# Performance work log

Hardware: AMD Instinct MI355X
Metric: run time of the kernel (lower is better)

Reference implementation:

```python
import jax, jax.numpy as jnp
import numpy as np

B, T, D = 4, 50, 512
SRC, SENTS, WORDS = 400, 16, 40
NEG = jnp.float32(-1e30)  # stands in for -inf mask fill (numerically identical post-softmax)


def _seq_mask(lengths, max_len):
    # [n, max_len] bool, True where position < length
    return jnp.arange(max_len)[None, :] < lengths[:, None]


def _mlp_score(q, h, Wq, bq, Uc, v):
    # Bahdanau additive score: v^T tanh(W q + U h)
    # q: [b,t,d], h: [b,s,d] -> [b,t,s]
    wq = q @ Wq + bq                       # [b,t,d]
    uh = h @ Uc                            # [b,s,d]
    wquh = jnp.tanh(wq[:, :, None, :] + uh[:, None, :, :])  # [b,t,s,d]
    return jnp.einsum('btsd,d->bts', wquh, v)


def setup_inputs() -> dict:
    key = jax.random.key(0)
    ks = jax.random.split(key, 20)
    s = np.float32(1.0 / np.sqrt(D))
    def p(k, shape):
        return jax.random.normal(k, shape, jnp.float32) * s
    return {
        'source': jax.random.normal(ks[0], (B, T, D), jnp.float32),
        'src_bank': jax.random.normal(ks[1], (SRC, B, D), jnp.float32),
        'src_lengths': jax.random.randint(ks[2], (B,), 1, SRC + 1),
        'qa_sent_bank': jax.random.normal(ks[3], (SENTS, B, D), jnp.float32),
        'qa_sent_lengths': jax.random.randint(ks[4], (B,), 1, SENTS + 1),
        'qa_word_bank': jax.random.normal(ks[5], (WORDS, B, SENTS, D), jnp.float32),
        'qa_word_lengths': jax.random.randint(ks[6], (B, SENTS), 1, WORDS + 1),
        'Wq_word': p(ks[7], (D, D)), 'bq_word': jnp.zeros((D,), jnp.float32),
        'Uc_word': p(ks[8], (D, D)), 'v_word': p(ks[9], (D,)),
        'Wq_sent': p(ks[10], (D, D)), 'bq_sent': jnp.zeros((D,), jnp.float32),
        'Uc_sent': p(ks[11], (D, D)), 'v_sent': p(ks[12], (D,)),
        'Wq_pass': p(ks[13], (D, D)), 'bq_pass': jnp.zeros((D,), jnp.float32),
        'Uc_pass': p(ks[14], (D, D)), 'v_pass': p(ks[15], (D,)),
    }


def _forward(source, src_bank, qa_sent_bank, qa_word_bank,
             Wq_word, bq_word, Uc_word, v_word,
             Wq_sent, bq_sent, Uc_sent, v_sent,
             Wq_pass, bq_pass, Uc_pass, v_pass,
             src_lengths, qa_word_lengths):
    b = source.shape[0]
    # [words,b,sents,d] -> [b,sents,words,d] -> [b, sents*words, d]
    qa_word = jnp.transpose(qa_word_bank, (1, 2, 0, 3)).reshape(b, SENTS * WORDS, D)
    src = jnp.transpose(src_bank, (1, 0, 2))       # [b,src,d]
    sent = jnp.transpose(qa_sent_bank, (1, 0, 2))  # [b,sents,d]

    qa_word_align = _mlp_score(source, qa_word, Wq_word, bq_word, Uc_word, v_word)  # [b,t,sents*words]
    src_align = _mlp_score(source, src, Wq_pass, bq_pass, Uc_pass, v_pass)          # [b,t,src]
    qa_sent_align = _mlp_score(source, sent, Wq_sent, bq_sent, Uc_sent, v_sent)     # [b,t,sents]

    # hierarchical combination: word score scaled by its sentence score
    qa_hier = (qa_word_align.reshape(b, T, SENTS, WORDS)
               * qa_sent_align[..., None]).reshape(b, T, SENTS * WORDS)

    align = jnp.concatenate([src_align, qa_hier], axis=-1)  # [b,t,src+sents*words]

    qa_mask = _seq_mask(qa_word_lengths.reshape(-1), WORDS).reshape(b, SENTS * WORDS)[:, None, :]
    src_mask = _seq_mask(src_lengths, SRC)[:, None, :]
    mask = jnp.concatenate([src_mask, qa_mask], axis=-1)

    align = jnp.where(mask, align, NEG)
    align_vectors = jax.nn.softmax(align, axis=-1)  # joint length-masked softmax

    memory = jnp.concatenate([src, qa_word], axis=1)          # [b, src+sents*words, d]
    c = jnp.einsum('bts,bsd->btd', align_vectors, memory)     # weighted context sum
    return c


def reference(source, src_bank, src_lengths, qa_sent_bank, qa_sent_lengths,
              qa_word_bank, qa_word_lengths,
              Wq_word, bq_word, Uc_word, v_word,
              Wq_sent, bq_sent, Uc_sent, v_sent,
              Wq_pass, bq_pass, Uc_pass, v_pass):
    # qa_sent_lengths is accepted but unused, matching the original forward()
    return _forward(source, src_bank, qa_sent_bank, qa_word_bank,
                    Wq_word, bq_word, Uc_word, v_word,
                    Wq_sent, bq_sent, Uc_sent, v_sent,
                    Wq_pass, bq_pass, Uc_pass, v_pass,
                    src_lengths, qa_word_lengths)
```

## Files before the change

kernel.cpp:

```cpp
#include <hip/hip_runtime.h>
#include <hip/hip_bf16.h>


#define B_    4
#define T_    50
#define D_    512
#define SRC_  400
#define SENTS_ 16
#define WORDS_ 40
#define NW_   640
#define NMEM_ 1040
#define NJOB_ 1056

#define C2L2E 2.8853900817779268f

typedef unsigned short ushort_t;
using s8v = __attribute__((ext_vector_type(8))) short;
using f4v = __attribute__((ext_vector_type(4))) float;

#define OFF_WQ_WORD 0
#define OFF_WQ_SENT 102400
#define OFF_WQ_PASS 204800
#define OFF_UH_SRC  307200
#define OFF_UH_WORD 1126400
#define OFF_UH_SENT 2437120
#define OFF_SC_SRC  2469888
#define OFF_SC_WORD 2549888
#define OFF_SC_SENT 2677888

__device__ __forceinline__ ushort_t f2b(float f) {
    __hip_bfloat16 h = __float2bfloat16(f);
    return *(ushort_t*)&h;
}

__global__ __launch_bounds__(256) void kA(
    const float* __restrict__ source, const float* __restrict__ src_bank,
    const float* __restrict__ qa_sent_bank, const float* __restrict__ qa_word_bank,
    const float* __restrict__ w0, const float* __restrict__ w1,
    const float* __restrict__ w2, const float* __restrict__ w3,
    const float* __restrict__ w4, const float* __restrict__ w5,
    const float* __restrict__ bq_word, const float* __restrict__ bq_sent,
    const float* __restrict__ bq_pass,
    float* __restrict__ wsf)
{
    __shared__ float smemf[4224];
    int bid = blockIdx.x;
    int tid = threadIdx.x;

    int z, rem;
    if (bid < 96)       { z = bid >> 5; rem = bid & 31; }
    else if (bid < 416) { z = 3; rem = bid - 96; }
    else if (bid < 616) { z = 4; rem = bid - 416; }
    else                { z = 5; rem = bid - 616; }
    int by = rem >> 3, bx = rem & 7;
    int M, atype; const float* bias; const float* W; float* C;
    switch (z) {
        case 0: M = 200;  atype = 0; bias = bq_word; W = w0; C = wsf + OFF_WQ_WORD; break;
        case 1: M = 200;  atype = 0; bias = bq_sent; W = w1; C = wsf + OFF_WQ_SENT; break;
        case 2: M = 200;  atype = 0; bias = bq_pass; W = w2; C = wsf + OFF_WQ_PASS; break;
        case 3: M = 2560; atype = 1; bias = nullptr; W = w3; C = wsf + OFF_UH_WORD; break;
        case 4: M = 1600; atype = 2; bias = nullptr; W = w4; C = wsf + OFF_UH_SRC;  break;
        default: M = 64;  atype = 3; bias = nullptr; W = w5; C = wsf + OFF_UH_SENT; break;
    }
    int m0 = by * 64, n0 = bx * 64;

    int lane = tid & 63, wvx = tid >> 6, quad = lane >> 4, l16 = lane & 15;
    int sm = tid >> 2, koff = (tid & 3) * 8;
    int rW = tid >> 3, cW = (tid & 7) * 8;
    int rWs = rW * 68 + (cW ^ (((rW >> 3) & 3) << 4));
    int nB = tid >> 2, kB8 = (tid & 3) * 8;
    int colp = nB ^ (((kB8 >> 3) & 3) << 4);

    short* At = (short*)smemf;
    short* Bt = (short*)(smemf + 1024);
    float* Wtmp = smemf + 2048;

    const float* arow = nullptr;
    {
        int rr = m0 + sm;
        if (rr < M) {
            if (atype == 0) arow = source + rr * D_;
            else if (atype == 1) { int b = rr / NW_; int j = rr - b * NW_;
                                   int se = j / WORDS_; int wd = j - se * WORDS_;
                                   arow = qa_word_bank + ((wd * B_ + b) * SENTS_ + se) * D_; }
            else if (atype == 2) { int b = rr / SRC_; int j = rr - b * SRC_;
                                   arow = src_bank + (j * B_ + b) * D_; }
            else                 { int b = rr >> 4; int s2 = rr & 15;
                                   arow = qa_sent_bank + (s2 * B_ + b) * D_; }
        }
    }
    const float* wbase = W + n0 + cW;

    auto loadA = [&](float* r, int kk) {
        if (arow) {
            float4 f0 = *(const float4*)(arow + kk * 32 + koff);
            float4 f1 = *(const float4*)(arow + kk * 32 + koff + 4);
            r[0]=f0.x; r[1]=f0.y; r[2]=f0.z; r[3]=f0.w;
            r[4]=f1.x; r[5]=f1.y; r[6]=f1.z; r[7]=f1.w;
        } else {
#pragma unroll
            for (int i = 0; i < 8; ++i) r[i] = 0.f;
        }
    };
    auto loadW = [&](float* r, int kk) {
        const float* p = wbase + (kk * 32 + rW) * D_;
        float4 f0 = *(const float4*)p;
        float4 f1 = *(const float4*)(p + 4);
        r[0]=f0.x; r[1]=f0.y; r[2]=f0.z; r[3]=f0.w;
        r[4]=f1.x; r[5]=f1.y; r[6]=f1.z; r[7]=f1.w;
    };
    auto storeWtmp = [&](const float* r) {
        *(float4*)(Wtmp + rWs)     = float4{r[0], r[1], r[2], r[3]};
        *(float4*)(Wtmp + rWs + 4) = float4{r[4], r[5], r[6], r[7]};
    };
    auto storeAt = [&](const float* r) {
        union { ushort_t u[8]; int4 v; } pk;
#pragma unroll
        for (int i = 0; i < 8; ++i) pk.u[i] = f2b(r[i]);
        *(int4*)(At + sm * 32 + koff) = pk.v;
    };
    auto buildBt = [&]() {
        union { ushort_t u[8]; int4 v; } pk;
#pragma unroll
        for (int i = 0; i < 8; ++i) pk.u[i] = f2b(Wtmp[(kB8 + i) * 68 + colp]);
        *(int4*)(Bt + nB * 32 + kB8) = pk.v;
    };

    f4v acc[4] = { {0.f,0.f,0.f,0.f}, {0.f,0.f,0.f,0.f},
                   {0.f,0.f,0.f,0.f}, {0.f,0.f,0.f,0.f} };

    float ac[8], an[8], wn[8];
    loadA(ac, 0);
    {
        float w0r[8];
        loadW(w0r, 0);
        storeWtmp(w0r);
    }
    loadW(wn, 1);
    loadA(an, 1);
    __syncthreads();

    for (int kk = 0; kk < 16; ++kk) {
        storeAt(ac);
        buildBt();
        __syncthreads();
        if (kk < 15) storeWtmp(wn);
        if (kk < 14) loadW(wn, kk + 2);
        if (kk < 15) {
#pragma unroll
            for (int i = 0; i < 8; ++i) ac[i] = an[i];
        }
        if (kk < 14) loadA(an, kk + 2);
        s8v af = *(const s8v*)(At + (wvx * 16 + l16) * 32 + quad * 8);
#pragma unroll
        for (int ng = 0; ng < 4; ++ng) {
            s8v bf = *(const s8v*)(Bt + (ng * 16 + l16) * 32 + quad * 8);
            acc[ng] = __builtin_amdgcn_mfma_f32_16x16x32_bf16(af, bf, acc[ng], 0, 0, 0);
        }
        __syncthreads();
    }

#pragma unroll
    for (int ng = 0; ng < 4; ++ng) {
        int col = n0 + ng * 16 + l16;
        float bb = bias ? bias[col] : 0.f;
#pragma unroll
        for (int rr2 = 0; rr2 < 4; ++rr2) {
            int row = m0 + wvx * 16 + quad * 4 + rr2;
            if (row < M) C[row * D_ + col] = (acc[ng][rr2] + bb) * C2L2E;
        }
    }
}

__global__ __launch_bounds__(256) void k2_scores(
    const float* __restrict__ v_word, const float* __restrict__ v_sent,
    const float* __restrict__ v_pass,
    const int* __restrict__ src_lengths, const int* __restrict__ qa_word_lengths,
    float* __restrict__ wsf)
{
    int lane = threadIdx.x & 63;
    int jid = blockIdx.x * 4 + (threadIdx.x >> 6);
    int job = jid / 5, fifth = jid - job * 5;
    int b = job / NJOB_, slot = job - b * NJOB_;
    const float* uh; const float* v; const float* wq; float* out; int ostride;
    if (slot < SRC_) {
        if (slot >= src_lengths[b]) return;
        uh = wsf + OFF_UH_SRC + (size_t)(b * SRC_ + slot) * D_;
        v = v_pass; wq = wsf + OFF_WQ_PASS + b * T_ * D_;
        out = wsf + OFF_SC_SRC + b * T_ * SRC_ + slot; ostride = SRC_;
    } else if (slot < NMEM_) {
        int j = slot - SRC_;
        int se = j / WORDS_; int wd = j - se * WORDS_;
        if (wd >= qa_word_lengths[b * SENTS_ + se]) return;
        uh = wsf + OFF_UH_WORD + (size_t)(b * NW_ + j) * D_;
        v = v_word; wq = wsf + OFF_WQ_WORD + b * T_ * D_;
        out = wsf + OFF_SC_WORD + b * T_ * NW_ + j; ostride = NW_;
    } else {
        int s2 = slot - NMEM_;
        uh = wsf + OFF_UH_SENT + (size_t)(b * SENTS_ + s2) * D_;
        v = v_sent; wq = wsf + OFF_WQ_SENT + b * T_ * D_;
        out = wsf + OFF_SC_SENT + b * T_ * SENTS_ + s2; ostride = SENTS_;
    }
    int d0 = lane * 8;
    float4 u0 = *(const float4*)(uh + d0);
    float4 u1 = *(const float4*)(uh + d0 + 4);
    float uhr[8] = {u0.x, u0.y, u0.z, u0.w, u1.x, u1.y, u1.z, u1.w};
    float4 v0 = *(const float4*)(v + d0);
    float4 v1 = *(const float4*)(v + d0 + 4);
    float vr[8] = {v0.x, v0.y, v0.z, v0.w, v1.x, v1.y, v1.z, v1.w};

    float vs = ((vr[0] + vr[1]) + (vr[2] + vr[3])) + ((vr[4] + vr[5]) + (vr[6] + vr[7]));
#pragma unroll
    for (int off = 32; off > 0; off >>= 1) vs += __shfl_xor(vs, off, 64);

    const float* wqh = wq + (fifth * 10) * D_ + d0;
    int tbase = fifth * 10;
#pragma unroll 1
    for (int g = 0; g < 2; ++g) {
        float a5[5];
#pragma unroll
        for (int u5 = 0; u5 < 5; ++u5) {
            const float* wr = wqh + (g * 5 + u5) * D_;
            float4 w0 = *(const float4*)(wr);
            float4 w1 = *(const float4*)(wr + 4);
            float wrr[8] = {w0.x, w0.y, w0.z, w0.w, w1.x, w1.y, w1.z, w1.w};
            float a = 0.f;
#pragma unroll
            for (int j = 0; j < 8; ++j) {
                float e = __builtin_amdgcn_exp2f(wrr[j] + uhr[j]);
                float r = __builtin_amdgcn_rcpf(e + 1.f);
                a = fmaf(vr[j], r, a);
            }
            a5[u5] = a;
        }
#pragma unroll
        for (int off = 32; off > 0; off >>= 1) {
#pragma unroll
            for (int u5 = 0; u5 < 5; ++u5) a5[u5] += __shfl_xor(a5[u5], off, 64);
        }
        if (lane == 0) {
#pragma unroll
            for (int u5 = 0; u5 < 5; ++u5)
                out[(tbase + g * 5 + u5) * ostride] = fmaf(-2.f, a5[u5], vs);
        }
    }
}

__global__ __launch_bounds__(256) void k3ac(
    const int* __restrict__ src_lengths, const int* __restrict__ qa_word_lengths,
    const float* __restrict__ wsf,
    const float* __restrict__ src_bank, const float* __restrict__ qa_word_bank,
    float* __restrict__ out)
{
    __shared__ float p[NMEM_];
    __shared__ float red[4];
    int tid = threadIdx.x, lane = tid & 63, wv = tid >> 6;
    int bt = blockIdx.x, b = bt / T_, t = bt - b * T_;
    const float* sc_src  = wsf + OFF_SC_SRC  + bt * SRC_;
    const float* sc_word = wsf + OFF_SC_WORD + bt * NW_;
    const float* sc_sent = wsf + OFF_SC_SENT + bt * SENTS_;
    int slen = src_lengths[b];

    float mx = -3.0e38f;
    for (int j = tid; j < NMEM_; j += 256) {
        float val;
        if (j < SRC_) {
            val = (j < slen) ? sc_src[j] : -1e30f;
        } else {
            int jj = j - SRC_; int se = jj / WORDS_; int wd = jj - se * WORDS_;
            float raw = sc_word[jj] * sc_sent[se];
            val = (wd < qa_word_lengths[b * SENTS_ + se]) ? raw : -1e30f;
        }
        p[j] = val;
        mx = fmaxf(mx, val);
    }
#pragma unroll
    for (int off = 32; off > 0; off >>= 1) mx = fmaxf(mx, __shfl_xor(mx, off, 64));
    if (lane == 0) red[wv] = mx;
    __syncthreads();
    mx = fmaxf(fmaxf(red[0], red[1]), fmaxf(red[2], red[3]));
    __syncthreads();
    float lsum = 0.f;
    for (int j = tid; j < NMEM_; j += 256) {
        float e = __expf(p[j] - mx);
        p[j] = e; lsum += e;
    }
#pragma unroll
    for (int off = 32; off > 0; off >>= 1) lsum += __shfl_xor(lsum, off, 64);
    if (lane == 0) red[wv] = lsum;
    __syncthreads();
    float inv = 1.f / (red[0] + red[1] + red[2] + red[3]);
    for (int j = tid; j < NMEM_; j += 256) p[j] *= inv;
    __syncthreads();

    int d0 = tid * 2;
    float acc0 = 0.f, acc1 = 0.f;
    {
        int slen4 = (slen + 3) & ~3;
        const float* bank = src_bank + (size_t)b * D_ + d0;
        for (int s = 0; s < slen4; s += 4) {
            float4 pv = *(const float4*)(p + s);
            const float* r0 = bank + (size_t)s * (B_ * D_);
            float2 m0 = *(const float2*)(r0);
            float2 m1 = *(const float2*)(r0 + B_ * D_);
            float2 m2 = *(const float2*)(r0 + 2 * B_ * D_);
            float2 m3 = *(const float2*)(r0 + 3 * B_ * D_);
            acc0 = fmaf(pv.x, m0.x, acc0); acc1 = fmaf(pv.x, m0.y, acc1);
            acc0 = fmaf(pv.y, m1.x, acc0); acc1 = fmaf(pv.y, m1.y, acc1);
            acc0 = fmaf(pv.z, m2.x, acc0); acc1 = fmaf(pv.z, m2.y, acc1);
            acc0 = fmaf(pv.w, m3.x, acc0); acc1 = fmaf(pv.w, m3.y, acc1);
        }
    }
#pragma unroll 1
    for (int se = 0; se < SENTS_; ++se) {
        int lim = qa_word_lengths[b * SENTS_ + se];
        int lim4 = (lim + 3) & ~3;
        const float* bank = qa_word_bank + ((size_t)b * SENTS_ + se) * D_ + d0;
        const float* pw = p + SRC_ + se * WORDS_;
        for (int wd = 0; wd < lim4; wd += 4) {
            float4 pv = *(const float4*)(pw + wd);
            const float* r0 = bank + (size_t)wd * (B_ * SENTS_ * D_);
            float2 m0 = *(const float2*)(r0);
            float2 m1 = *(const float2*)(r0 + B_ * SENTS_ * D_);
            float2 m2 = *(const float2*)(r0 + 2 * B_ * SENTS_ * D_);
            float2 m3 = *(const float2*)(r0 + 3 * B_ * SENTS_ * D_);
            acc0 = fmaf(pv.x, m0.x, acc0); acc1 = fmaf(pv.x, m0.y, acc1);
            acc0 = fmaf(pv.y, m1.x, acc0); acc1 = fmaf(pv.y, m1.y, acc1);
            acc0 = fmaf(pv.z, m2.x, acc0); acc1 = fmaf(pv.z, m2.y, acc1);
            acc0 = fmaf(pv.w, m3.x, acc0); acc1 = fmaf(pv.w, m3.y, acc1);
        }
    }
    *(float2*)(out + (size_t)(b * T_ + t) * D_ + d0) = float2{acc0, acc1};
}

extern "C" void kernel_launch(void* const* d_in, const int* in_sizes, int n_in,
                              void* d_out, int out_size, void* d_ws, size_t ws_size,
                              hipStream_t stream)
{
    (void)in_sizes; (void)n_in; (void)out_size; (void)ws_size;
    const float* source          = (const float*)d_in[0];
    const float* src_bank        = (const float*)d_in[1];
    const int*   src_lengths     = (const int*)d_in[2];
    const float* qa_sent_bank    = (const float*)d_in[3];
    const float* qa_word_bank    = (const float*)d_in[5];
    const int*   qa_word_lengths = (const int*)d_in[6];
    const float* Wq_word = (const float*)d_in[7];
    const float* bq_word = (const float*)d_in[8];
    const float* Uc_word = (const float*)d_in[9];
    const float* v_word  = (const float*)d_in[10];
    const float* Wq_sent = (const float*)d_in[11];
    const float* bq_sent = (const float*)d_in[12];
    const float* Uc_sent = (const float*)d_in[13];
    const float* v_sent  = (const float*)d_in[14];
    const float* Wq_pass = (const float*)d_in[15];
    const float* bq_pass = (const float*)d_in[16];
    const float* Uc_pass = (const float*)d_in[17];
    const float* v_pass  = (const float*)d_in[18];

    float* wsf = (float*)d_ws;
    float* out = (float*)d_out;

    kA<<<dim3(624), dim3(256), 0, stream>>>(
        source, src_bank, qa_sent_bank, qa_word_bank,
        Wq_word, Wq_sent, Wq_pass, Uc_word, Uc_pass, Uc_sent,
        bq_word, bq_sent, bq_pass, wsf);
    k2_scores<<<dim3(5280), dim3(256), 0, stream>>>(
        v_word, v_sent, v_pass, src_lengths, qa_word_lengths, wsf);
    k3ac<<<dim3(200), dim3(256), 0, stream>>>(
        src_lengths, qa_word_lengths, wsf, src_bank, qa_word_bank, out);
}
```

Baseline: 188.3 us.

## Split context kernel across D quarters and memory halves with prefetched gemv

The context-sum kernel now launches four blocks per (b,t) row, each covering 128 output dims, and splits the memory rows between two half-blocks whose partial sums are combined through shared memory. The inner loop is rewritten as an 8-row software-pipelined gemv that prefetches the next bank rows and probabilities. The aim is more parallelism and memory-level concurrency on the bandwidth-bound weighted sum, which previously ran on only 200 blocks. In exchange, every block recomputes the softmax over 1040 entries, and rounding row counts up to multiples of 8 adds reads of masked rows that carry zero weight.

```diff
diff --git a/kernel.cpp b/kernel.cpp
--- a/kernel.cpp
+++ b/kernel.cpp
@@ -253,9 +253,12 @@
     float* __restrict__ out)
 {
     __shared__ float p[NMEM_];
+    __shared__ float part[256];
     __shared__ float red[4];
     int tid = threadIdx.x, lane = tid & 63, wv = tid >> 6;
-    int bt = blockIdx.x, b = bt / T_, t = bt - b * T_;
+    int bid = blockIdx.x;
+    int bt = bid >> 2, dq = bid & 3;
+    int b = bt / T_, t = bt - b * T_;
     const float* sc_src  = wsf + OFF_SC_SRC  + bt * SRC_;
     const float* sc_word = wsf + OFF_SC_WORD + bt * NW_;
     const float* sc_sent = wsf + OFF_SC_SENT + bt * SENTS_;
@@ -293,44 +296,56 @@
     for (int j = tid; j < NMEM_; j += 256) p[j] *= inv;
     __syncthreads();
 
-    int d0 = tid * 2;
-    float acc0 = 0.f, acc1 = 0.f;
+    int c = tid & 127, sh = tid >> 7;
+    int d = dq * 128 + c;
+    float acc = 0.f;
+
+    auto gemv8 = [&](const float* bank, int strd, const float* pseg, int r0, int r1) {
+        if (r0 >= r1) return;
+        const float* rp = bank + (size_t)r0 * strd;
+        float m0 = rp[0], m1 = rp[strd], m2 = rp[2*strd], m3 = rp[3*strd];
+        float m4 = rp[4*strd], m5 = rp[5*strd], m6 = rp[6*strd], m7 = rp[7*strd];
+        float4 pa = *(const float4*)(pseg + r0);
+        float4 pb = *(const float4*)(pseg + r0 + 4);
+        for (int r = r0; r + 8 < r1; r += 8) {
+            const float* np = bank + (size_t)(r + 8) * strd;
+            float n0 = np[0], n1 = np[strd], n2 = np[2*strd], n3 = np[3*strd];
+            float n4 = np[4*strd], n5 = np[5*strd], n6 = np[6*strd], n7 = np[7*strd];
+            float4 qa = *(const float4*)(pseg + r + 8);
+            float4 qb = *(const float4*)(pseg + r + 12);
+            acc = fmaf(pa.x, m0, acc); acc = fmaf(pa.y, m1, acc);
+            acc = fmaf(pa.z, m2, acc); acc = fmaf(pa.w, m3, acc);
+            acc = fmaf(pb.x, m4, acc); acc = fmaf(pb.y, m5, acc);
+            acc = fmaf(pb.z, m6, acc); acc = fmaf(pb.w, m7, acc);
+            m0 = n0; m1 = n1; m2 = n2; m3 = n3;
+            m4 = n4; m5 = n5; m6 = n6; m7 = n7;
+            pa = qa; pb = qb;
+        }
+        acc = fmaf(pa.x, m0, acc); acc = fmaf(pa.y, m1, acc);
+        acc = fmaf(pa.z, m2, acc); acc = fmaf(pa.w, m3, acc);
+        acc = fmaf(pb.x, m4, acc); acc = fmaf(pb.y, m5, acc);
+        acc = fmaf(pb.z, m6, acc); acc = fmaf(pb.w, m7, acc);
+    };
+
     {
-        int slen4 = (slen + 3) & ~3;
-        const float* bank = src_bank + (size_t)b * D_ + d0;
-        for (int s = 0; s < slen4; s += 4) {
-            float4 pv = *(const float4*)(p + s);
-            const float* r0 = bank + (size_t)s * (B_ * D_);
-            float2 m0 = *(const float2*)(r0);
-            float2 m1 = *(const float2*)(r0 + B_ * D_);
-            float2 m2 = *(const float2*)(r0 + 2 * B_ * D_);
-            float2 m3 = *(const float2*)(r0 + 3 * B_ * D_);
-            acc0 = fmaf(pv.x, m0.x, acc0); acc1 = fmaf(pv.x, m0.y, acc1);
-            acc0 = fmaf(pv.y, m1.x, acc0); acc1 = fmaf(pv.y, m1.y, acc1);
-            acc0 = fmaf(pv.z, m2.x, acc0); acc1 = fmaf(pv.z, m2.y, acc1);
-            acc0 = fmaf(pv.w, m3.x, acc0); acc1 = fmaf(pv.w, m3.y, acc1);
-        }
+        int slen8 = (slen + 7) & ~7;
+        const float* bank = src_bank + (size_t)b * D_ + d;
+        int s0 = (sh == 0) ? 0 : 200;
+        int s1 = (sh == 0) ? min(slen8, 200) : slen8;
+        gemv8(bank, B_ * D_, p, s0, s1);
     }
 #pragma unroll 1
-    for (int se = 0; se < SENTS_; ++se) {
+    for (int se = sh * 8; se < sh * 8 + 8; ++se) {
         int lim = qa_word_lengths[b * SENTS_ + se];
-        int lim4 = (lim + 3) & ~3;
-        const float* bank = qa_word_bank + ((size_t)b * SENTS_ + se) * D_ + d0;
-        const float* pw = p + SRC_ + se * WORDS_;
-        for (int wd = 0; wd < lim4; wd += 4) {
-            float4 pv = *(const float4*)(pw + wd);
-            const float* r0 = bank + (size_t)wd * (B_ * SENTS_ * D_);
-            float2 m0 = *(const float2*)(r0);
-            float2 m1 = *(const float2*)(r0 + B_ * SENTS_ * D_);
-            float2 m2 = *(const float2*)(r0 + 2 * B_ * SENTS_ * D_);
-            float2 m3 = *(const float2*)(r0 + 3 * B_ * SENTS_ * D_);
-            acc0 = fmaf(pv.x, m0.x, acc0); acc1 = fmaf(pv.x, m0.y, acc1);
-            acc0 = fmaf(pv.y, m1.x, acc0); acc1 = fmaf(pv.y, m1.y, acc1);
-            acc0 = fmaf(pv.z, m2.x, acc0); acc1 = fmaf(pv.z, m2.y, acc1);
-            acc0 = fmaf(pv.w, m3.x, acc0); acc1 = fmaf(pv.w, m3.y, acc1);
-        }
-    }
-    *(float2*)(out + (size_t)(b * T_ + t) * D_ + d0) = float2{acc0, acc1};
+        int lim8 = (lim + 7) & ~7;
+        const float* bank = qa_word_bank + ((size_t)b * SENTS_ + se) * D_ + d;
+        gemv8(bank, B_ * SENTS_ * D_, p + SRC_ + se * WORDS_, 0, lim8);
+    }
+
+    part[tid] = acc;
+    __syncthreads();
+    if (tid < 128)
+        out[(size_t)(b * T_ + t) * D_ + dq * 128 + tid] = part[tid] + part[tid + 128];
 }
 
 extern "C" void kernel_launch(void* const* d_in, const int* in_sizes, int n_in,
@@ -366,6 +381,6 @@
         bq_word, bq_sent, bq_pass, wsf);
     k2_scores<<<dim3(5280), dim3(256), 0, stream>>>(
         v_word, v_sent, v_pass, src_lengths, qa_word_lengths, wsf);
-    k3ac<<<dim3(200), dim3(256), 0, stream>>>(
+    k3ac<<<dim3(800), dim3(256), 0, stream>>>(
         src_lengths, qa_word_lengths, wsf, src_bank, qa_word_bank, out);
 }
```

Result: faster. 159.4 us (-15.4%).
